# Kernel tuning notes

Hardware: AMD Instinct MI355X
Metric: run time of the kernel (lower is better)

The kernel has to match this reference:

```python
import jax, jax.numpy as jnp
import numpy as np

B, X_DIM, Z_DIM, K = 16384, 784, 64, 64
LOG2PI = 1.8378770664093453


def setup_inputs() -> dict:
    key = jax.random.key(0)
    ks = jax.random.split(key, 8)
    pi_raw = jax.random.uniform(ks[1], (B, K), dtype=jnp.float32) + 1e-3
    pi = pi_raw / jnp.sum(pi_raw, axis=1, keepdims=True)
    return {
        "x": jax.random.normal(ks[0], (B, X_DIM), dtype=jnp.float32),
        "pi": pi,
        "qz_mu": jax.random.normal(ks[2], (B, Z_DIM), dtype=jnp.float32),
        "qz_logsigma": 0.5 * jax.random.normal(ks[3], (B, Z_DIM), dtype=jnp.float32),
        "eps": jax.random.normal(ks[4], (B, Z_DIM), dtype=jnp.float32),
        "pz_y_mu": jax.random.normal(ks[5], (K, Z_DIM), dtype=jnp.float32),
        "pz_y_logsigma": jnp.zeros((K, Z_DIM), dtype=jnp.float32),  # log(init_sigma=1.0)
        "W_dec": jax.random.normal(ks[6], (Z_DIM, X_DIM), dtype=jnp.float32) / np.sqrt(Z_DIM),
        "b_dec": jnp.zeros((X_DIM,), dtype=jnp.float32),
    }


def reference(x, pi, qz_mu, qz_logsigma, eps, pz_y_mu, pz_y_logsigma, W_dec, b_dec):
    # GMMVAE.elbo with num_samples=1; rsample reparameterized with fixed eps.
    qs = jnp.exp(qz_logsigma)                      # [B, z]
    z = qz_mu + qs * eps                           # [B, z]

    # log p(x | z): unit-variance Gaussian likelihood with linear decoder
    mean = z @ W_dec + b_dec                       # [B, x]
    log_px_z = jnp.sum(-0.5 * (x - mean) ** 2 - 0.5 * LOG2PI)

    # py_z: vectorized over all k components (fuses the original Python loop)
    ps = jnp.exp(pz_y_logsigma)                    # [k, z]
    diff = z[:, None, :] - pz_y_mu[None, :, :]     # [B, k, z]
    comp_lp = jnp.sum(-0.5 * (diff / ps[None]) ** 2 - pz_y_logsigma[None] - 0.5 * LOG2PI, axis=-1)  # [B, k]
    log_pi = jnp.log(pi)
    pzy = comp_lp + log_pi                         # [B, k]
    log_py_z = pzy - jax.scipy.special.logsumexp(pzy, axis=1, keepdims=True)
    probs = jnp.exp(log_py_z)                      # [B, k]

    # kl_y = sum_b KL(Cat(py_z) || Cat(pi))
    kl_y = jnp.sum(probs * (log_py_z - log_pi))

    # kl_z = sum_b sum_k probs[b,k] * KL(N(qz_mu, qs) || N(mu_k, ps_k)).sum(z)
    mdiff = qz_mu[:, None, :] - pz_y_mu[None, :, :]  # [B, k, z]
    klz_bk = jnp.sum(
        pz_y_logsigma[None] - qz_logsigma[:, None, :]
        + (qs[:, None, :] ** 2 + mdiff ** 2) / (2.0 * ps[None] ** 2)
        - 0.5,
        axis=-1,
    )                                              # [B, k]
    kl_z = jnp.sum(probs * klz_bk)

    elbo = (log_px_z - kl_y - kl_z) / x.shape[0]
    return elbo
```

## Files before the change

kernel.cpp:

```cpp
#include <hip/hip_runtime.h>

#define NB 16384
#define XD 784
#define ZD 64
#define KK 64
#define LOG2PI_F 1.8378770664093453f
#define LDA 72

typedef __attribute__((ext_vector_type(8))) short short8;
typedef __attribute__((ext_vector_type(4))) float floatx4;


__device__ __forceinline__ float wave_sum(float x) {
    #pragma unroll
    for (int o = 32; o > 0; o >>= 1) x += __shfl_xor(x, o, 64);
    return x;
}

__device__ __forceinline__ unsigned short f2bf(float f) {
    unsigned u = __float_as_uint(f);
    unsigned r = (u + 0x7FFF + ((u >> 16) & 1)) >> 16;
    return (unsigned short)r;
}

__device__ __forceinline__ unsigned int pack2(float a, float b) {
    return (unsigned int)f2bf(a) | ((unsigned int)f2bf(b) << 16);
}

__global__ __launch_bounds__(256) void prep_kernel(
    const float* __restrict__ W, const float* __restrict__ pmu_g,
    const float* __restrict__ plog_g,
    unsigned short* __restrict__ Wt, unsigned short* __restrict__ Bi2_g,
    unsigned short* __restrict__ Bm1_g, float* __restrict__ Sk_g,
    float* __restrict__ Gk_g, float* __restrict__ Ck_g)
{
    const int tid = threadIdx.x;
    const int b = blockIdx.x;
    if (b < 196) {
        int idx = b * 256 + tid;
        int k = idx / XD;
        int n = idx - k * XD;
        Wt[n * ZD + k] = f2bf(W[idx]);
    } else {
        const int k = tid >> 2;
        const int q = tid & 3;
        const int v0 = q * 16;
        const int gb = k * 64 + v0;
        float s = 0.f, g = 0.f;
        unsigned int* pi2 = (unsigned int*)&Bi2_g[k * 64 + v0];
        unsigned int* pm1 = (unsigned int*)&Bm1_g[k * 64 + v0];
        #pragma unroll
        for (int i = 0; i < 4; ++i) {
            float4 mu4 = *(const float4*)&pmu_g[gb + 4 * i];
            float4 lg4 = *(const float4*)&plog_g[gb + 4 * i];
            float m0[4] = {mu4.x, mu4.y, mu4.z, mu4.w};
            float l0[4] = {lg4.x, lg4.y, lg4.z, lg4.w};
            float i2v[4], m1v[4];
            #pragma unroll
            for (int j = 0; j < 4; ++j) {
                float i2 = 0.5f * __expf(-2.f * l0[j]);
                i2v[j] = i2;
                m1v[j] = m0[j] * i2;
                g = fmaf(m0[j] * m0[j], i2, g);
                s += l0[j];
            }
            pi2[i * 2 + 0] = pack2(i2v[0], i2v[1]);
            pi2[i * 2 + 1] = pack2(i2v[2], i2v[3]);
            pm1[i * 2 + 0] = pack2(m1v[0], m1v[1]);
            pm1[i * 2 + 1] = pack2(m1v[2], m1v[3]);
        }
        s += __shfl_xor(s, 1, 64);
        s += __shfl_xor(s, 2, 64);
        g += __shfl_xor(g, 1, 64);
        g += __shfl_xor(g, 2, 64);
        if (q == 0) {
            Sk_g[k] = s;
            Gk_g[k] = g;
            Ck_g[k] = -s - 32.0f * LOG2PI_F;
        }
    }
}

__global__ __launch_bounds__(256) void fused_kernel(
    const float* __restrict__ x, const float* __restrict__ pi,
    const float* __restrict__ qmu, const float* __restrict__ qls,
    const float* __restrict__ eps,
    const unsigned short* __restrict__ Wt, const float* __restrict__ bd,
    const unsigned short* __restrict__ Bi2_g, const unsigned short* __restrict__ Bm1_g,
    const float* __restrict__ Sk_g, const float* __restrict__ Gk_g,
    const float* __restrict__ Ck_g,
    float* __restrict__ dec_p, float* __restrict__ kly_p, float* __restrict__ klz_p)
{
    __shared__ unsigned short Az[16 * LDA];
    __shared__ unsigned short Az2[16 * LDA];
    __shared__ unsigned short Azm[16 * LDA];
    __shared__ unsigned short Aq2[16 * LDA];
    __shared__ unsigned short Aqm[16 * LDA];
    __shared__ float Sk_s[64], Gk_s[64], Ck_s[64], sql_s[16];
    __shared__ float MxP[4][16], SxP[4][16];
    __shared__ float r1[4], r2[4], rs[4];

    const int tid = threadIdx.x;
    const int row0 = blockIdx.x * 16;

    {
        const int r = tid >> 4;
        const int c = (tid & 15) * 4;
        const int gb = (row0 + r) * 64 + c;
        float4 mu4 = *(const float4*)&qmu[gb];
        float4 ls4 = *(const float4*)&qls[gb];
        float4 ep4 = *(const float4*)&eps[gb];
        float m0[4] = {mu4.x, mu4.y, mu4.z, mu4.w};
        float l0[4] = {ls4.x, ls4.y, ls4.z, ls4.w};
        float e0[4] = {ep4.x, ep4.y, ep4.z, ep4.w};
        float z[4], q2[4], sls = 0.f;
        #pragma unroll
        for (int j = 0; j < 4; ++j) {
            float qs = __expf(l0[j]);
            z[j] = fmaf(qs, e0[j], m0[j]);
            q2[j] = fmaf(m0[j], m0[j], qs * qs);
            sls += l0[j];
        }
        unsigned* pa = (unsigned*)&Az[r * LDA + c];
        pa[0] = pack2(z[0], z[1]);               pa[1] = pack2(z[2], z[3]);
        unsigned* pb = (unsigned*)&Az2[r * LDA + c];
        pb[0] = pack2(z[0] * z[0], z[1] * z[1]); pb[1] = pack2(z[2] * z[2], z[3] * z[3]);
        unsigned* pc = (unsigned*)&Azm[r * LDA + c];
        pc[0] = pack2(-2.f * z[0], -2.f * z[1]); pc[1] = pack2(-2.f * z[2], -2.f * z[3]);
        unsigned* pd = (unsigned*)&Aq2[r * LDA + c];
        pd[0] = pack2(q2[0], q2[1]);             pd[1] = pack2(q2[2], q2[3]);
        unsigned* pe = (unsigned*)&Aqm[r * LDA + c];
        pe[0] = pack2(-2.f * m0[0], -2.f * m0[1]); pe[1] = pack2(-2.f * m0[2], -2.f * m0[3]);
        sls += __shfl_xor(sls, 1, 64);
        sls += __shfl_xor(sls, 2, 64);
        sls += __shfl_xor(sls, 4, 64);
        sls += __shfl_xor(sls, 8, 64);
        if ((tid & 15) == 0) sql_s[r] = sls;
        if (tid < 64) {
            Sk_s[tid] = Sk_g[tid];
            Gk_s[tid] = Gk_g[tid];
            Ck_s[tid] = Ck_g[tid];
        }
    }
    __syncthreads();

    const int lane = tid & 63;
    const int w    = tid >> 6;
    const int m    = lane & 15;
    const int quad = lane >> 4;
    const int kk   = w * 16 + m;

    floatx4 ca = {0.f, 0.f, 0.f, 0.f}, cc = {0.f, 0.f, 0.f, 0.f};
    {
        const short8 az2_0 = *(const short8*)&Az2[m * LDA + quad * 8];
        const short8 az2_1 = *(const short8*)&Az2[m * LDA + 32 + quad * 8];
        const short8 azm_0 = *(const short8*)&Azm[m * LDA + quad * 8];
        const short8 azm_1 = *(const short8*)&Azm[m * LDA + 32 + quad * 8];
        const short8 aq2_0 = *(const short8*)&Aq2[m * LDA + quad * 8];
        const short8 aq2_1 = *(const short8*)&Aq2[m * LDA + 32 + quad * 8];
        const short8 aqm_0 = *(const short8*)&Aqm[m * LDA + quad * 8];
        const short8 aqm_1 = *(const short8*)&Aqm[m * LDA + 32 + quad * 8];
        const short8 bi0 = *(const short8*)&Bi2_g[kk * 64 + quad * 8];
        const short8 bi1 = *(const short8*)&Bi2_g[kk * 64 + 32 + quad * 8];
        const short8 bm0 = *(const short8*)&Bm1_g[kk * 64 + quad * 8];
        const short8 bm1 = *(const short8*)&Bm1_g[kk * 64 + 32 + quad * 8];
        ca = __builtin_amdgcn_mfma_f32_16x16x32_bf16(az2_0, bi0, ca, 0, 0, 0);
        ca = __builtin_amdgcn_mfma_f32_16x16x32_bf16(az2_1, bi1, ca, 0, 0, 0);
        ca = __builtin_amdgcn_mfma_f32_16x16x32_bf16(azm_0, bm0, ca, 0, 0, 0);
        ca = __builtin_amdgcn_mfma_f32_16x16x32_bf16(azm_1, bm1, ca, 0, 0, 0);
        cc = __builtin_amdgcn_mfma_f32_16x16x32_bf16(aq2_0, bi0, cc, 0, 0, 0);
        cc = __builtin_amdgcn_mfma_f32_16x16x32_bf16(aq2_1, bi1, cc, 0, 0, 0);
        cc = __builtin_amdgcn_mfma_f32_16x16x32_bf16(aqm_0, bm0, cc, 0, 0, 0);
        cc = __builtin_amdgcn_mfma_f32_16x16x32_bf16(aqm_1, bm1, cc, 0, 0, 0);
    }

    const float ckv = Ck_s[kk], gkv = Gk_s[kk], skv = Sk_s[kk];
    float comp[4], ev[4], mxw[4], sw[4];
    #pragma unroll
    for (int r = 0; r < 4; ++r) {
        comp[r] = ckv - (ca[r] + gkv);
        float pzv = comp[r] + __logf(pi[(row0 + quad * 4 + r) * 64 + kk]);
        float mx = pzv;
        #pragma unroll
        for (int o = 1; o <= 8; o <<= 1) mx = fmaxf(mx, __shfl_xor(mx, o, 64));
        float e = __expf(pzv - mx);
        float s = e;
        #pragma unroll
        for (int o = 1; o <= 8; o <<= 1) s += __shfl_xor(s, o, 64);
        mxw[r] = mx; sw[r] = s; ev[r] = e;
    }
    if (m == 0) {
        #pragma unroll
        for (int r = 0; r < 4; ++r) {
            MxP[w][quad * 4 + r] = mxw[r];
            SxP[w][quad * 4 + r] = sw[r];
        }
    }
    __syncthreads();

    float kly = 0.f, klz = 0.f;
    #pragma unroll
    for (int r = 0; r < 4; ++r) {
        const int row = quad * 4 + r;
        float g0 = MxP[0][row], g1 = MxP[1][row], g2 = MxP[2][row], g3 = MxP[3][row];
        float gmx = fmaxf(fmaxf(g0, g1), fmaxf(g2, g3));
        float st = SxP[0][row] * __expf(g0 - gmx) + SxP[1][row] * __expf(g1 - gmx)
                 + SxP[2][row] * __expf(g2 - gmx) + SxP[3][row] * __expf(g3 - gmx);
        float lse = gmx + __logf(st);
        float p = ev[r] * __expf(mxw[r] - gmx) * __frcp_rn(st);
        kly = fmaf(p, comp[r] - lse, kly);
        klz = fmaf(p, skv - sql_s[row] + cc[r] + gkv - 32.0f, klz);
    }
    kly = wave_sum(kly);
    klz = wave_sum(klz);
    if (lane == 0) { r1[w] = kly; r2[w] = klz; }

    const short8 af0 = *(const short8*)&Az[m * LDA + quad * 8];
    const short8 af1 = *(const short8*)&Az[m * LDA + 32 + quad * 8];
    const int xrow = (row0 + quad * 4) * XD;

    float xa0, xa1, xa2, xa3, bb;
    short8 w0, w1;
    {
        const int col = w * 16 + m;
        xa0 = x[xrow + 0 * XD + col];
        xa1 = x[xrow + 1 * XD + col];
        xa2 = x[xrow + 2 * XD + col];
        xa3 = x[xrow + 3 * XD + col];
        bb  = bd[col];
        w0  = *(const short8*)&Wt[col * 64 + quad * 8];
        w1  = *(const short8*)&Wt[col * 64 + 32 + quad * 8];
    }

    float accl = 0.f;
    #pragma unroll 1
    for (int t = w; t < 49; t += 4) {
        const float cx0 = xa0, cx1 = xa1, cx2 = xa2, cx3 = xa3, cb = bb;
        const short8 cw0 = w0, cw1 = w1;
        const int tn = t + 4;
        if (tn < 49) {
            const int col = tn * 16 + m;
            xa0 = x[xrow + 0 * XD + col];
            xa1 = x[xrow + 1 * XD + col];
            xa2 = x[xrow + 2 * XD + col];
            xa3 = x[xrow + 3 * XD + col];
            bb  = bd[col];
            w0  = *(const short8*)&Wt[col * 64 + quad * 8];
            w1  = *(const short8*)&Wt[col * 64 + 32 + quad * 8];
        }
        floatx4 c = {0.f, 0.f, 0.f, 0.f};
        c = __builtin_amdgcn_mfma_f32_16x16x32_bf16(af0, cw0, c, 0, 0, 0);
        c = __builtin_amdgcn_mfma_f32_16x16x32_bf16(af1, cw1, c, 0, 0, 0);
        float d0 = cx0 - (c[0] + cb);
        float d1 = cx1 - (c[1] + cb);
        float d2 = cx2 - (c[2] + cb);
        float d3 = cx3 - (c[3] + cb);
        accl = fmaf(d0, d0, accl);
        accl = fmaf(d1, d1, accl);
        accl = fmaf(d2, d2, accl);
        accl = fmaf(d3, d3, accl);
    }

    float sdec = wave_sum(accl);
    if (lane == 0) rs[w] = sdec;
    __syncthreads();
    if (tid == 0) {
        dec_p[blockIdx.x] = -0.5f * (rs[0] + rs[1] + rs[2] + rs[3]);
        kly_p[blockIdx.x] = r1[0] + r1[1] + r1[2] + r1[3];
        klz_p[blockIdx.x] = r2[0] + r2[1] + r2[2] + r2[3];
    }
}

__global__ __launch_bounds__(256) void finalize_kernel(
    const float* __restrict__ dec_p, const float* __restrict__ kly_p,
    const float* __restrict__ klz_p, float* __restrict__ out)
{
    __shared__ double s0[256], s1[256], s2[256];
    const int tid = threadIdx.x;
    double a0 = 0.0, a1 = 0.0, a2 = 0.0;
    for (int i = tid; i < 1024; i += 256) {
        a0 += (double)dec_p[i];
        a1 += (double)kly_p[i];
        a2 += (double)klz_p[i];
    }
    s0[tid] = a0; s1[tid] = a1; s2[tid] = a2;
    __syncthreads();
    #pragma unroll
    for (int off = 128; off > 0; off >>= 1) {
        if (tid < off) {
            s0[tid] += s0[tid + off];
            s1[tid] += s1[tid + off];
            s2[tid] += s2[tid + off];
        }
        __syncthreads();
    }
    if (tid == 0) {
        double lpx = s0[0] - 0.5 * 1.8378770664093453 * (double)NB * (double)XD;
        out[0] = (float)((lpx - s1[0] - s2[0]) / (double)NB);
    }
}

extern "C" void kernel_launch(void* const* d_in, const int* in_sizes, int n_in,
                              void* d_out, int out_size, void* d_ws, size_t ws_size,
                              hipStream_t stream) {
    const float* x    = (const float*)d_in[0];
    const float* pi   = (const float*)d_in[1];
    const float* qmu  = (const float*)d_in[2];
    const float* qls  = (const float*)d_in[3];
    const float* eps  = (const float*)d_in[4];
    const float* pmu  = (const float*)d_in[5];
    const float* plog = (const float*)d_in[6];
    const float* W    = (const float*)d_in[7];
    const float* bd   = (const float*)d_in[8];
    float* out = (float*)d_out;

    char* wsb = (char*)d_ws;
    unsigned short* Wt   = (unsigned short*)(wsb);
    unsigned short* Bi2g = (unsigned short*)(wsb + 100352);
    unsigned short* Bm1g = (unsigned short*)(wsb + 108544);
    float* Skg   = (float*)(wsb + 116736);
    float* Gkg   = (float*)(wsb + 116992);
    float* Ckg   = (float*)(wsb + 117248);
    float* dec_p = (float*)(wsb + 117504);
    float* kly_p = (float*)(wsb + 121600);
    float* klz_p = (float*)(wsb + 125696);

    prep_kernel<<<197, 256, 0, stream>>>(W, pmu, plog, Wt, Bi2g, Bm1g, Skg, Gkg, Ckg);
    fused_kernel<<<NB / 16, 256, 0, stream>>>(x, pi, qmu, qls, eps, Wt, bd,
                                              Bi2g, Bm1g, Skg, Gkg, Ckg,
                                              dec_p, kly_p, klz_p);
    finalize_kernel<<<1, 256, 0, stream>>>(dec_p, kly_p, klz_p, out);
}
```

Before: 126.2 us.

## Fuse finalize reduction into main kernel via last-block atomic counter

Removes the separate finalize kernel launch. The last block to finish, detected with an atomic counter that prep_kernel resets, now performs the double-precision reduction. It also loads pi with vectorized float4 reads and precomputes log(pi) into shared memory instead of doing scattered per-lane global loads. The first x tile loads are hoisted ahead of the barrier so they overlap the MFMA stage. The cost is extra shared memory (about 6KB of double reduction buffers plus the Lpi tile), which may reduce occupancy, and an added fence and atomic per block.

```diff
diff --git a/kernel.cpp b/kernel.cpp
--- a/kernel.cpp
+++ b/kernel.cpp
@@ -32,7 +32,8 @@
     const float* __restrict__ plog_g,
     unsigned short* __restrict__ Wt, unsigned short* __restrict__ Bi2_g,
     unsigned short* __restrict__ Bm1_g, float* __restrict__ Sk_g,
-    float* __restrict__ Gk_g, float* __restrict__ Ck_g)
+    float* __restrict__ Gk_g, float* __restrict__ Ck_g,
+    unsigned int* __restrict__ counter)
 {
     const int tid = threadIdx.x;
     const int b = blockIdx.x;
@@ -78,6 +79,7 @@
             Gk_g[k] = g;
             Ck_g[k] = -s - 32.0f * LOG2PI_F;
         }
+        if (tid == 0) *counter = 0u;
     }
 }
 
@@ -89,16 +91,20 @@
     const unsigned short* __restrict__ Bi2_g, const unsigned short* __restrict__ Bm1_g,
     const float* __restrict__ Sk_g, const float* __restrict__ Gk_g,
     const float* __restrict__ Ck_g,
-    float* __restrict__ dec_p, float* __restrict__ kly_p, float* __restrict__ klz_p)
+    float* __restrict__ dec_p, float* __restrict__ kly_p, float* __restrict__ klz_p,
+    unsigned int* __restrict__ counter, float* __restrict__ out)
 {
     __shared__ unsigned short Az[16 * LDA];
     __shared__ unsigned short Az2[16 * LDA];
     __shared__ unsigned short Azm[16 * LDA];
     __shared__ unsigned short Aq2[16 * LDA];
     __shared__ unsigned short Aqm[16 * LDA];
+    __shared__ float Lpi[16][68];
     __shared__ float Sk_s[64], Gk_s[64], Ck_s[64], sql_s[16];
     __shared__ float MxP[4][16], SxP[4][16];
     __shared__ float r1[4], r2[4], rs[4];
+    __shared__ unsigned int lastf;
+    __shared__ double sred0[256], sred1[256], sred2[256];
 
     const int tid = threadIdx.x;
     const int row0 = blockIdx.x * 16;
@@ -110,6 +116,7 @@
         float4 mu4 = *(const float4*)&qmu[gb];
         float4 ls4 = *(const float4*)&qls[gb];
         float4 ep4 = *(const float4*)&eps[gb];
+        float4 pi4 = *(const float4*)&pi[gb];
         float m0[4] = {mu4.x, mu4.y, mu4.z, mu4.w};
         float l0[4] = {ls4.x, ls4.y, ls4.z, ls4.w};
         float e0[4] = {ep4.x, ep4.y, ep4.z, ep4.w};
@@ -131,6 +138,10 @@
         pd[0] = pack2(q2[0], q2[1]);             pd[1] = pack2(q2[2], q2[3]);
         unsigned* pe = (unsigned*)&Aqm[r * LDA + c];
         pe[0] = pack2(-2.f * m0[0], -2.f * m0[1]); pe[1] = pack2(-2.f * m0[2], -2.f * m0[3]);
+        float4 lp4;
+        lp4.x = __logf(pi4.x); lp4.y = __logf(pi4.y);
+        lp4.z = __logf(pi4.z); lp4.w = __logf(pi4.w);
+        *(float4*)&Lpi[r][c] = lp4;
         sls += __shfl_xor(sls, 1, 64);
         sls += __shfl_xor(sls, 2, 64);
         sls += __shfl_xor(sls, 4, 64);
@@ -142,7 +153,6 @@
             Ck_s[tid] = Ck_g[tid];
         }
     }
-    __syncthreads();
 
     const int lane = tid & 63;
     const int w    = tid >> 6;
@@ -150,28 +160,48 @@
     const int quad = lane >> 4;
     const int kk   = w * 16 + m;
 
+    const int xrow = (row0 + quad * 4) * XD;
+    float xa0, xa1, xa2, xa3, bb;
+    {
+        const int col = w * 16 + m;
+        xa0 = x[xrow + 0 * XD + col];
+        xa1 = x[xrow + 1 * XD + col];
+        xa2 = x[xrow + 2 * XD + col];
+        xa3 = x[xrow + 3 * XD + col];
+        bb  = bd[col];
+    }
+    __syncthreads();
+
     floatx4 ca = {0.f, 0.f, 0.f, 0.f}, cc = {0.f, 0.f, 0.f, 0.f};
     {
-        const short8 az2_0 = *(const short8*)&Az2[m * LDA + quad * 8];
-        const short8 az2_1 = *(const short8*)&Az2[m * LDA + 32 + quad * 8];
-        const short8 azm_0 = *(const short8*)&Azm[m * LDA + quad * 8];
-        const short8 azm_1 = *(const short8*)&Azm[m * LDA + 32 + quad * 8];
-        const short8 aq2_0 = *(const short8*)&Aq2[m * LDA + quad * 8];
-        const short8 aq2_1 = *(const short8*)&Aq2[m * LDA + 32 + quad * 8];
-        const short8 aqm_0 = *(const short8*)&Aqm[m * LDA + quad * 8];
-        const short8 aqm_1 = *(const short8*)&Aqm[m * LDA + 32 + quad * 8];
         const short8 bi0 = *(const short8*)&Bi2_g[kk * 64 + quad * 8];
         const short8 bi1 = *(const short8*)&Bi2_g[kk * 64 + 32 + quad * 8];
         const short8 bm0 = *(const short8*)&Bm1_g[kk * 64 + quad * 8];
         const short8 bm1 = *(const short8*)&Bm1_g[kk * 64 + 32 + quad * 8];
-        ca = __builtin_amdgcn_mfma_f32_16x16x32_bf16(az2_0, bi0, ca, 0, 0, 0);
-        ca = __builtin_amdgcn_mfma_f32_16x16x32_bf16(az2_1, bi1, ca, 0, 0, 0);
-        ca = __builtin_amdgcn_mfma_f32_16x16x32_bf16(azm_0, bm0, ca, 0, 0, 0);
-        ca = __builtin_amdgcn_mfma_f32_16x16x32_bf16(azm_1, bm1, ca, 0, 0, 0);
-        cc = __builtin_amdgcn_mfma_f32_16x16x32_bf16(aq2_0, bi0, cc, 0, 0, 0);
-        cc = __builtin_amdgcn_mfma_f32_16x16x32_bf16(aq2_1, bi1, cc, 0, 0, 0);
-        cc = __builtin_amdgcn_mfma_f32_16x16x32_bf16(aqm_0, bm0, cc, 0, 0, 0);
-        cc = __builtin_amdgcn_mfma_f32_16x16x32_bf16(aqm_1, bm1, cc, 0, 0, 0);
+        {
+            const short8 a0 = *(const short8*)&Az2[m * LDA + quad * 8];
+            const short8 a1 = *(const short8*)&Az2[m * LDA + 32 + quad * 8];
+            ca = __builtin_amdgcn_mfma_f32_16x16x32_bf16(a0, bi0, ca, 0, 0, 0);
+            ca = __builtin_amdgcn_mfma_f32_16x16x32_bf16(a1, bi1, ca, 0, 0, 0);
+        }
+        {
+            const short8 a0 = *(const short8*)&Aq2[m * LDA + quad * 8];
+            const short8 a1 = *(const short8*)&Aq2[m * LDA + 32 + quad * 8];
+            cc = __builtin_amdgcn_mfma_f32_16x16x32_bf16(a0, bi0, cc, 0, 0, 0);
+            cc = __builtin_amdgcn_mfma_f32_16x16x32_bf16(a1, bi1, cc, 0, 0, 0);
+        }
+        {
+            const short8 a0 = *(const short8*)&Azm[m * LDA + quad * 8];
+            const short8 a1 = *(const short8*)&Azm[m * LDA + 32 + quad * 8];
+            ca = __builtin_amdgcn_mfma_f32_16x16x32_bf16(a0, bm0, ca, 0, 0, 0);
+            ca = __builtin_amdgcn_mfma_f32_16x16x32_bf16(a1, bm1, ca, 0, 0, 0);
+        }
+        {
+            const short8 a0 = *(const short8*)&Aqm[m * LDA + quad * 8];
+            const short8 a1 = *(const short8*)&Aqm[m * LDA + 32 + quad * 8];
+            cc = __builtin_amdgcn_mfma_f32_16x16x32_bf16(a0, bm0, cc, 0, 0, 0);
+            cc = __builtin_amdgcn_mfma_f32_16x16x32_bf16(a1, bm1, cc, 0, 0, 0);
+        }
     }
 
     const float ckv = Ck_s[kk], gkv = Gk_s[kk], skv = Sk_s[kk];
@@ -179,7 +209,7 @@
     #pragma unroll
     for (int r = 0; r < 4; ++r) {
         comp[r] = ckv - (ca[r] + gkv);
-        float pzv = comp[r] + __logf(pi[(row0 + quad * 4 + r) * 64 + kk]);
+        float pzv = comp[r] + Lpi[quad * 4 + r][kk];
         float mx = pzv;
         #pragma unroll
         for (int o = 1; o <= 8; o <<= 1) mx = fmaxf(mx, __shfl_xor(mx, o, 64));
@@ -217,19 +247,11 @@
 
     const short8 af0 = *(const short8*)&Az[m * LDA + quad * 8];
     const short8 af1 = *(const short8*)&Az[m * LDA + 32 + quad * 8];
-    const int xrow = (row0 + quad * 4) * XD;
-
-    float xa0, xa1, xa2, xa3, bb;
     short8 w0, w1;
     {
         const int col = w * 16 + m;
-        xa0 = x[xrow + 0 * XD + col];
-        xa1 = x[xrow + 1 * XD + col];
-        xa2 = x[xrow + 2 * XD + col];
-        xa3 = x[xrow + 3 * XD + col];
-        bb  = bd[col];
-        w0  = *(const short8*)&Wt[col * 64 + quad * 8];
-        w1  = *(const short8*)&Wt[col * 64 + 32 + quad * 8];
+        w0 = *(const short8*)&Wt[col * 64 + quad * 8];
+        w1 = *(const short8*)&Wt[col * 64 + 32 + quad * 8];
     }
 
     float accl = 0.f;
@@ -264,39 +286,43 @@
     float sdec = wave_sum(accl);
     if (lane == 0) rs[w] = sdec;
     __syncthreads();
+
     if (tid == 0) {
         dec_p[blockIdx.x] = -0.5f * (rs[0] + rs[1] + rs[2] + rs[3]);
         kly_p[blockIdx.x] = r1[0] + r1[1] + r1[2] + r1[3];
         klz_p[blockIdx.x] = r2[0] + r2[1] + r2[2] + r2[3];
-    }
-}
-
-__global__ __launch_bounds__(256) void finalize_kernel(
-    const float* __restrict__ dec_p, const float* __restrict__ kly_p,
-    const float* __restrict__ klz_p, float* __restrict__ out)
-{
-    __shared__ double s0[256], s1[256], s2[256];
-    const int tid = threadIdx.x;
-    double a0 = 0.0, a1 = 0.0, a2 = 0.0;
-    for (int i = tid; i < 1024; i += 256) {
-        a0 += (double)dec_p[i];
-        a1 += (double)kly_p[i];
-        a2 += (double)klz_p[i];
-    }
-    s0[tid] = a0; s1[tid] = a1; s2[tid] = a2;
+        __threadfence();
+        unsigned int t = __hip_atomic_fetch_add(counter, 1u, __ATOMIC_ACQ_REL,
+                                                __HIP_MEMORY_SCOPE_AGENT);
+        lastf = (t == (unsigned int)(gridDim.x - 1)) ? 1u : 0u;
+    }
     __syncthreads();
-    #pragma unroll
-    for (int off = 128; off > 0; off >>= 1) {
-        if (tid < off) {
-            s0[tid] += s0[tid + off];
-            s1[tid] += s1[tid + off];
-            s2[tid] += s2[tid + off];
-        }
+    if (lastf) {
+        __threadfence();
+        const volatile float* dp = (const volatile float*)dec_p;
+        const volatile float* yp = (const volatile float*)kly_p;
+        const volatile float* zp = (const volatile float*)klz_p;
+        double a0 = 0.0, a1 = 0.0, a2 = 0.0;
+        for (int i = tid; i < 1024; i += 256) {
+            a0 += (double)dp[i];
+            a1 += (double)yp[i];
+            a2 += (double)zp[i];
+        }
+        sred0[tid] = a0; sred1[tid] = a1; sred2[tid] = a2;
         __syncthreads();
-    }
-    if (tid == 0) {
-        double lpx = s0[0] - 0.5 * 1.8378770664093453 * (double)NB * (double)XD;
-        out[0] = (float)((lpx - s1[0] - s2[0]) / (double)NB);
+        #pragma unroll
+        for (int off = 128; off > 0; off >>= 1) {
+            if (tid < off) {
+                sred0[tid] += sred0[tid + off];
+                sred1[tid] += sred1[tid + off];
+                sred2[tid] += sred2[tid + off];
+            }
+            __syncthreads();
+        }
+        if (tid == 0) {
+            double lpx = sred0[0] - 0.5 * 1.8378770664093453 * (double)NB * (double)XD;
+            out[0] = (float)((lpx - sred1[0] - sred2[0]) / (double)NB);
+        }
     }
 }
 
@@ -324,10 +350,10 @@
     float* dec_p = (float*)(wsb + 117504);
     float* kly_p = (float*)(wsb + 121600);
     float* klz_p = (float*)(wsb + 125696);
-
-    prep_kernel<<<197, 256, 0, stream>>>(W, pmu, plog, Wt, Bi2g, Bm1g, Skg, Gkg, Ckg);
+    unsigned int* counter = (unsigned int*)(wsb + 129792);
+
+    prep_kernel<<<197, 256, 0, stream>>>(W, pmu, plog, Wt, Bi2g, Bm1g, Skg, Gkg, Ckg, counter);
     fused_kernel<<<NB / 16, 256, 0, stream>>>(x, pi, qmu, qls, eps, Wt, bd,
                                               Bi2g, Bm1g, Skg, Gkg, Ckg,
-                                              dec_p, kly_p, klz_p);
-    finalize_kernel<<<1, 256, 0, stream>>>(dec_p, kly_p, klz_p, out);
-}
+                                              dec_p, kly_p, klz_p, counter, out);
+}
```

Measured after the change: 176.5 us. 1.4x slower.
